# Kernel optimization log

Hardware: AMD Instinct MI355X
Metric: run time of the kernel (lower is better)

Reference implementation:

```python
import jax, jax.numpy as jnp
import numpy as np

EPS = 1e-5  # BatchNorm2d default eps


def setup_inputs() -> dict:
    key = jax.random.key(0)
    ks = jax.random.split(key, 6)
    N, C_in, C_out, H, W = 32, 64, 32, 224, 224
    return {
        "x": jax.random.normal(ks[0], (N, C_in, H, W), dtype=jnp.float32),
        "conv_w": jax.random.normal(ks[1], (C_out, C_in), dtype=jnp.float32) * 0.1,
        "gamma": jax.random.uniform(ks[2], (C_in,), dtype=jnp.float32, minval=0.5, maxval=1.5),
        "beta": jax.random.normal(ks[3], (C_in,), dtype=jnp.float32) * 0.1,
        "running_mean": jax.random.normal(ks[4], (C_in,), dtype=jnp.float32) * 0.1,
        "running_var": jax.random.uniform(ks[5], (C_in,), dtype=jnp.float32, minval=0.5, maxval=1.5),
    }


def reference(x, conv_w, gamma, beta, running_mean, running_var):
    # Inference BN folded to per-channel affine: y = x * scale + bias
    scale = gamma / jnp.sqrt(running_var + EPS)          # [C_in]
    bias = beta - running_mean * scale                   # [C_in]
    y = jnp.maximum(x * scale[None, :, None, None] + bias[None, :, None, None], 0.0)
    # 1x1 conv: contract over input channels. [N,C_in,H,W] x [C_out,C_in] -> [N,C_out,H,W]
    z = jnp.einsum("nchw,oc->nohw", y, conv_w)
    # 2x2 average pool, stride 2
    N, C_out, H, W = z.shape
    z = z.reshape(N, C_out, H // 2, 2, W // 2, 2).mean(axis=(3, 5))
    return z
```

## Files before the change

### kernel.cpp

```cpp
#include <hip/hip_runtime.h>
#include <hip/hip_bf16.h>


#define EPS_BN 1e-5f

typedef float v2f __attribute__((ext_vector_type(2)));

constexpr int N_   = 32;
constexpr int CIN  = 64;
constexpr int COUT = 32;
constexpr int H_   = 224;
constexpr int W_   = 224;
constexpr int H2   = 112;
constexpr int W2   = 112;
constexpr int PIX  = N_ * H2 * W2;
constexpr int BLK  = 256;

__global__ void prep_kernel(const float* __restrict__ conv_w,
                            const float* __restrict__ gamma,
                            const float* __restrict__ beta,
                            const float* __restrict__ rmean,
                            const float* __restrict__ rvar,
                            float* __restrict__ ws) {
    int j = blockIdx.x * blockDim.x + threadIdx.x;
    if (j < CIN * COUT) {
        int c = j >> 5, o = j & 31;
        ws[2 * CIN + j] = conv_w[o * CIN + c];
    }
    if (j < CIN) {
        float s = gamma[j] * rsqrtf(rvar[j] + EPS_BN);
        float b = beta[j] - rmean[j] * s;
        ws[j]       = 0.25f * s;
        ws[CIN + j] = 0.25f * b;
    }
}

__global__ __launch_bounds__(BLK, 5) void fused_kernel(const float* __restrict__ x,
                                                       const float* __restrict__ ws,
                                                       float* __restrict__ out) {
    const float* __restrict__ sc = ws;
    const float* __restrict__ bi = ws + CIN;
    const float* __restrict__ wT = ws + 2 * CIN;

    int i = blockIdx.x * BLK + threadIdx.x;
    int n  = i / (H2 * W2);
    int r  = i - n * (H2 * W2);
    int h2 = r / W2;
    int w2 = r - h2 * W2;

    const float* __restrict__ px =
        x + ((size_t)n * CIN * H_ + (size_t)(2 * h2)) * W_ + (size_t)(2 * w2);

    float acc[COUT];
#pragma unroll
    for (int o = 0; o < COUT; ++o) acc[o] = 0.0f;

#pragma unroll 8
    for (int c = 0; c < CIN; ++c) {
        const float* p = px + (size_t)c * (H_ * W_);
        v2f r0 = __builtin_nontemporal_load(reinterpret_cast<const v2f*>(p));
        v2f r1 = __builtin_nontemporal_load(reinterpret_cast<const v2f*>(p + W_));
        float s = sc[c];
        float b = bi[c];
        float y = fmaxf(fmaf(r0.x, s, b), 0.0f)
                + fmaxf(fmaf(r0.y, s, b), 0.0f)
                + fmaxf(fmaf(r1.x, s, b), 0.0f)
                + fmaxf(fmaf(r1.y, s, b), 0.0f);
#pragma unroll
        for (int o = 0; o < COUT; ++o)
            acc[o] = fmaf(wT[c * COUT + o], y, acc[o]);
    }

    float* __restrict__ po = out + ((size_t)n * COUT * H2 + (size_t)h2) * W2 + (size_t)w2;
#pragma unroll
    for (int o = 0; o < COUT; ++o)
        __builtin_nontemporal_store(acc[o], po + (size_t)o * (H2 * W2));
}

extern "C" void kernel_launch(void* const* d_in, const int* in_sizes, int n_in,
                              void* d_out, int out_size, void* d_ws, size_t ws_size,
                              hipStream_t stream) {
    const float* x      = (const float*)d_in[0];
    const float* conv_w = (const float*)d_in[1];
    const float* gamma  = (const float*)d_in[2];
    const float* beta   = (const float*)d_in[3];
    const float* rmean  = (const float*)d_in[4];
    const float* rvar   = (const float*)d_in[5];
    float* out = (float*)d_out;
    float* ws  = (float*)d_ws;

    prep_kernel<<<(CIN * COUT + BLK - 1) / BLK, BLK, 0, stream>>>(
        conv_w, gamma, beta, rmean, rvar, ws);
    fused_kernel<<<PIX / BLK, BLK, 0, stream>>>(x, ws, out);
}
```

Before: 87.39 us.

## Double-buffer channel loads with explicit prefetch and schedule barriers

Restructures the channel loop so each thread loads eight channels into one register buffer while it computes on the other buffer. Schedule barriers pin the loads ahead of the compute, so more memory requests are in flight per wave. Address arithmetic moves to 32-bit offsets. The larger register footprint comes with a lower occupancy bound in the launch bounds, which may reduce the number of waves available to hide latency.

```diff
diff --git a/kernel.cpp b/kernel.cpp
--- a/kernel.cpp
+++ b/kernel.cpp
@@ -1,5 +1,4 @@
 #include <hip/hip_runtime.h>
-#include <hip/hip_bf16.h>
 
 
 #define EPS_BN 1e-5f
@@ -15,6 +14,7 @@
 constexpr int W2   = 112;
 constexpr int PIX  = N_ * H2 * W2;
 constexpr int BLK  = 256;
+constexpr int CHK  = 8;
 
 __global__ void prep_kernel(const float* __restrict__ conv_w,
                             const float* __restrict__ gamma,
@@ -35,7 +35,7 @@
     }
 }
 
-__global__ __launch_bounds__(BLK, 5) void fused_kernel(const float* __restrict__ x,
+__global__ __launch_bounds__(BLK, 4) void fused_kernel(const float* __restrict__ x,
                                                        const float* __restrict__ ws,
                                                        float* __restrict__ out) {
     const float* __restrict__ sc = ws;
@@ -48,27 +48,46 @@
     int h2 = r / W2;
     int w2 = r - h2 * W2;
 
-    const float* __restrict__ px =
-        x + ((size_t)n * CIN * H_ + (size_t)(2 * h2)) * W_ + (size_t)(2 * w2);
+    uint32_t base = ((uint32_t)(n * CIN) * H_ + (uint32_t)(2 * h2)) * W_ + 2 * w2;
 
     float acc[COUT];
 #pragma unroll
     for (int o = 0; o < COUT; ++o) acc[o] = 0.0f;
 
-#pragma unroll 8
-    for (int c = 0; c < CIN; ++c) {
-        const float* p = px + (size_t)c * (H_ * W_);
-        v2f r0 = __builtin_nontemporal_load(reinterpret_cast<const v2f*>(p));
-        v2f r1 = __builtin_nontemporal_load(reinterpret_cast<const v2f*>(p + W_));
-        float s = sc[c];
-        float b = bi[c];
-        float y = fmaxf(fmaf(r0.x, s, b), 0.0f)
-                + fmaxf(fmaf(r0.y, s, b), 0.0f)
-                + fmaxf(fmaf(r1.x, s, b), 0.0f)
-                + fmaxf(fmaf(r1.y, s, b), 0.0f);
+    v2f bufA[2 * CHK], bufB[2 * CHK];
+
+    auto LOAD = [&](v2f* buf, int c0) {
 #pragma unroll
-        for (int o = 0; o < COUT; ++o)
-            acc[o] = fmaf(wT[c * COUT + o], y, acc[o]);
+        for (int c = 0; c < CHK; ++c) {
+            uint32_t off = base + (uint32_t)(c0 + c) * (H_ * W_);
+            buf[2 * c]     = __builtin_nontemporal_load(reinterpret_cast<const v2f*>(x + off));
+            buf[2 * c + 1] = __builtin_nontemporal_load(reinterpret_cast<const v2f*>(x + off + W_));
+        }
+    };
+    auto COMP = [&](const v2f* buf, int c0) {
+#pragma unroll
+        for (int c = 0; c < CHK; ++c) {
+            float s = sc[c0 + c];
+            float b = bi[c0 + c];
+            v2f r0 = buf[2 * c], r1 = buf[2 * c + 1];
+            float y = fmaxf(fmaf(r0.x, s, b), 0.0f) + fmaxf(fmaf(r0.y, s, b), 0.0f)
+                    + fmaxf(fmaf(r1.x, s, b), 0.0f) + fmaxf(fmaf(r1.y, s, b), 0.0f);
+#pragma unroll
+            for (int o = 0; o < COUT; ++o)
+                acc[o] = fmaf(wT[(c0 + c) * COUT + o], y, acc[o]);
+        }
+    };
+
+    LOAD(bufA, 0);
+#pragma unroll
+    for (int q = 0; q < CIN / (2 * CHK); ++q) {
+        const int c0 = q * 2 * CHK;
+        LOAD(bufB, c0 + CHK);
+        __builtin_amdgcn_sched_barrier(0);
+        COMP(bufA, c0);
+        if (c0 + 2 * CHK < CIN) LOAD(bufA, c0 + 2 * CHK);
+        __builtin_amdgcn_sched_barrier(0);
+        COMP(bufB, c0 + CHK);
     }
 
     float* __restrict__ po = out + ((size_t)n * COUT * H2 + (size_t)h2) * W2 + (size_t)w2;
```

Measured after the change: 300.6 us. 3.44x slower.
